# Kernel tuning notes

Measured on AMD Instinct MI355X. Metric: run time of the kernel, lower is better.

The kernel has to match this reference:

```python
import jax, jax.numpy as jnp
import numpy as np

B, Q, C = 16, 2048, 256
SCORE_THRESH = 0.05   # lowered from 0.7 so the mask is non-trivial with 256 classes
NMS_THRESH = 0.7
LABEL_OFFSET = 1e5    # batched_nms trick: offset boxes per class so cross-class IoU ~ 0


def box_cxcywh_to_xyxy(b):
    cx, cy, w, h = jnp.split(b, 4, axis=-1)
    return jnp.concatenate([cx - 0.5 * w, cy - 0.5 * h, cx + 0.5 * w, cy + 0.5 * h], axis=-1)


def pairwise_iou(boxes):
    # boxes: [N,4] xyxy -> iou: [N,N]
    area = jnp.clip(boxes[:, 2] - boxes[:, 0], 0) * jnp.clip(boxes[:, 3] - boxes[:, 1], 0)
    lt = jnp.maximum(boxes[:, None, :2], boxes[None, :, :2])
    rb = jnp.minimum(boxes[:, None, 2:], boxes[None, :, 2:])
    wh = jnp.clip(rb - lt, 0)
    inter = wh[..., 0] * wh[..., 1]
    union = area[:, None] + area[None, :] - inter
    return inter / jnp.maximum(union, 1e-6)


def nms_single(boxes, scores, labels, valid):
    # Emulates torchvision batched_nms with fixed-size (padded) output:
    # returns score-sorted boxes/scores/labels plus a boolean keep mask.
    n = boxes.shape[0]
    boxes_off = boxes + labels.astype(boxes.dtype)[:, None] * LABEL_OFFSET
    order = jnp.argsort(jnp.where(valid, scores, -jnp.inf))[::-1]
    b_off = boxes_off[order]
    s = scores[order]
    l = labels[order]
    v = valid[order]
    iou = pairwise_iou(b_off)  # [N,N], class-offset so only same-class overlap
    idx = jnp.arange(n)

    def step(keep, x):
        row, i = x  # row: iou of box i vs all
        sup = (row > NMS_THRESH) & (idx > i) & keep[i]
        return keep & ~sup, None

    keep, _ = jax.lax.scan(step, v, (iou, idx))
    return boxes[order], s, l, keep & v


def setup_inputs() -> dict:
    key = jax.random.key(0)
    k1, k2, k3 = jax.random.split(key, 3)
    pred_logits = jax.random.normal(k1, (B, Q, C), dtype=jnp.float32)
    pred_boxes = jax.random.uniform(k2, (B, Q, 4), dtype=jnp.float32)
    target_sizes = jax.random.randint(k3, (B, 2), 480, 1333, dtype=jnp.int32)
    return {"pred_logits": pred_logits, "pred_boxes": pred_boxes, "target_sizes": target_sizes}


def reference(pred_logits, pred_boxes, target_sizes):
    prob = jax.nn.softmax(pred_logits, axis=-1)
    cls_prob = prob[..., :-1]            # drop 'no-object' class
    scores = cls_prob.max(axis=-1)       # [B,Q]
    labels = cls_prob.argmax(axis=-1)    # [B,Q]
    boxes = box_cxcywh_to_xyxy(pred_boxes)
    ts = target_sizes.astype(boxes.dtype)
    img_h, img_w = ts[:, 0], ts[:, 1]
    scale = jnp.stack([img_w, img_h, img_w, img_h], axis=1)  # [B,4]
    boxes = boxes * scale[:, None, :]
    valid = scores >= SCORE_THRESH
    out_boxes, out_scores, out_labels, keep = jax.vmap(nms_single)(boxes, scores, labels, valid)
    return out_boxes, out_scores, out_labels, keep
```

## Files before the change

kernel.cpp:

```cpp
#include <hip/hip_runtime.h>
#include <math.h>

#define NB 16
#define BQ 2048
#define NC 256
#define NL 255

typedef unsigned long long u64;
typedef unsigned int u32;
typedef unsigned short u16;
typedef unsigned char u8;

__device__ __forceinline__ u32 ord_f32(float f) {
  u32 b = __float_as_uint(f);
  return (b & 0x80000000u) ? ~b : (b | 0x80000000u);
}

__global__ __launch_bounds__(256) void score_box_kernel(
    const float* __restrict__ logits,
    const float* __restrict__ pboxes,
    const int* __restrict__ tsz,
    float* __restrict__ out)
{
#pragma clang fp contract(off)
  const int lane = threadIdx.x & 63;
  const int g = lane & 15;
  const int wv = threadIdx.x >> 6;
  const int q = (blockIdx.x * 4 + wv) * 4 + (lane >> 4);
  const float* row = logits + (size_t)q * NC + g * 16;
  const float4 la = *reinterpret_cast<const float4*>(row);
  const float4 lb4 = *reinterpret_cast<const float4*>(row + 4);
  const float4 lc = *reinterpret_cast<const float4*>(row + 8);
  const float4 ld = *reinterpret_cast<const float4*>(row + 12);

  float m = fmaxf(fmaxf(fmaxf(la.x, la.y), fmaxf(la.z, la.w)),
           fmaxf(fmaxf(fmaxf(lb4.x, lb4.y), fmaxf(lb4.z, lb4.w)),
           fmaxf(fmaxf(fmaxf(lc.x, lc.y), fmaxf(lc.z, lc.w)),
                 fmaxf(fmaxf(ld.x, ld.y), fmaxf(ld.z, ld.w)))));
  #pragma unroll
  for (int d = 1; d < 16; d <<= 1) m = fmaxf(m, __shfl_xor(m, d));

  float4 ea, eb, ec, ed;
  ea.x = expf(la.x - m);  ea.y = expf(la.y - m);  ea.z = expf(la.z - m);  ea.w = expf(la.w - m);
  eb.x = expf(lb4.x - m); eb.y = expf(lb4.y - m); eb.z = expf(lb4.z - m); eb.w = expf(lb4.w - m);
  ec.x = expf(lc.x - m);  ec.y = expf(lc.y - m);  ec.z = expf(lc.z - m);  ec.w = expf(lc.w - m);
  ed.x = expf(ld.x - m);  ed.y = expf(ld.y - m);  ed.z = expf(ld.z - m);  ed.w = expf(ld.w - m);

  float s = (((ea.x + ea.y) + (ea.z + ea.w)) + ((eb.x + eb.y) + (eb.z + eb.w)))
          + (((ec.x + ec.y) + (ec.z + ec.w)) + ((ed.x + ed.y) + (ed.z + ed.w)));
  #pragma unroll
  for (int d = 1; d < 16; d <<= 1) s += __shfl_xor(s, d);

  const int c0 = g * 16;
  float bp = ea.x / s; int bc = c0;
  float p;
  p = ea.y / s; if (p > bp) { bp = p; bc = c0 + 1; }
  p = ea.z / s; if (p > bp) { bp = p; bc = c0 + 2; }
  p = ea.w / s; if (p > bp) { bp = p; bc = c0 + 3; }
  p = eb.x / s; if (p > bp) { bp = p; bc = c0 + 4; }
  p = eb.y / s; if (p > bp) { bp = p; bc = c0 + 5; }
  p = eb.z / s; if (p > bp) { bp = p; bc = c0 + 6; }
  p = eb.w / s; if (p > bp) { bp = p; bc = c0 + 7; }
  p = ec.x / s; if (p > bp) { bp = p; bc = c0 + 8; }
  p = ec.y / s; if (p > bp) { bp = p; bc = c0 + 9; }
  p = ec.z / s; if (p > bp) { bp = p; bc = c0 + 10; }
  p = ec.w / s; if (p > bp) { bp = p; bc = c0 + 11; }
  p = ed.x / s; if (p > bp) { bp = p; bc = c0 + 12; }
  p = ed.y / s; if (p > bp) { bp = p; bc = c0 + 13; }
  p = ed.z / s; if (p > bp) { bp = p; bc = c0 + 14; }
  p = ed.w / s; if (g != 15 && p > bp) { bp = p; bc = c0 + 15; }
  #pragma unroll
  for (int d = 1; d < 16; d <<= 1) {
    const float op = __shfl_xor(bp, d);
    const int   oc = __shfl_xor(bc, d);
    if (op > bp || (op == bp && oc < bc)) { bp = op; bc = oc; }
  }

  if (g == 0) {
    const int b = q >> 11;
    float hf = (float)tsz[b * 2 + 0];
    float wf = (float)tsz[b * 2 + 1];
    float4 pb = *reinterpret_cast<const float4*>(pboxes + (size_t)q * 4);
    float hw = 0.5f * pb.z, hh = 0.5f * pb.w;
    float4 ob;
    ob.x = (pb.x - hw) * wf;
    ob.y = (pb.y - hh) * hf;
    ob.z = (pb.x + hw) * wf;
    ob.w = (pb.y + hh) * hf;
    *reinterpret_cast<float4*>(out + (size_t)q * 4) = ob;
    out[NB * BQ * 4 + q] = bp;
    out[NB * BQ * 5 + q] = (float)bc;
  }
}

__global__ __launch_bounds__(1024) void sort_nms_kernel(float* __restrict__ out)
{
#pragma clang fp contract(off)
  __shared__ __align__(16) u64 cvk[BQ];
  __shared__ u32 cgt_a[BQ];
  __shared__ float4 bx[BQ];
  __shared__ float4 bxo[BQ];
  __shared__ float scr[BQ];
  __shared__ u8 lb[BQ];
  __shared__ u8 lbp[BQ];
  __shared__ u8 kp[BQ];
  __shared__ u16 sidx[BQ];
  __shared__ u16 gpos[BQ];
  __shared__ u16 hist[32 * 256];
  __shared__ u32 tot[256];
  __shared__ u32 scn[256];
  __shared__ u32 wval[16], winv[16];

  const int b = blockIdx.x;
  const int tid = threadIdx.x;
  const int lane = tid & 63;
  const int wv = tid >> 6;
  float* boxes_g  = out + (size_t)b * BQ * 4;
  float* scores_g = out + NB * BQ * 4 + (size_t)b * BQ;
  float* labels_g = out + NB * BQ * 5 + (size_t)b * BQ;
  float* keep_g   = out + NB * BQ * 6 + (size_t)b * BQ;

  const int q0 = 2 * tid;
  float2 s2 = *reinterpret_cast<const float2*>(scores_g + q0);
  float2 lf = *reinterpret_cast<const float2*>(labels_g + q0);
  float4 bb0 = *reinterpret_cast<const float4*>(boxes_g + (size_t)q0 * 4);
  float4 bb1 = *reinterpret_cast<const float4*>(boxes_g + (size_t)q0 * 4 + 4);
  scr[q0] = s2.x; scr[q0 + 1] = s2.y;
  const u32 l0 = (u32)(int)lf.x, l1 = (u32)(int)lf.y;
  lb[q0] = (u8)l0; lb[q0 + 1] = (u8)l1;
  bx[q0] = bb0; bx[q0 + 1] = bb1;
  cgt_a[tid] = 0; cgt_a[tid + 1024] = 0;
  reinterpret_cast<u32*>(hist)[tid]        = 0;
  reinterpret_cast<u32*>(hist)[tid + 1024] = 0;
  reinterpret_cast<u32*>(hist)[tid + 2048] = 0;
  reinterpret_cast<u32*>(hist)[tid + 3072] = 0;
  const bool v0 = (s2.x >= 0.05f), v1 = (s2.y >= 0.05f);
  const u64 f0 = ((u64)(v0 ? ord_f32(s2.x) : 0x007FFFFFu) << 32) | ((u32)q0 << 8) | l0;
  const u64 f1 = ((u64)(v1 ? ord_f32(s2.y) : 0x007FFFFFu) << 32) | ((u32)(q0 + 1) << 8) | l1;
  const u64 b0 = __ballot(v0), b1 = __ballot(v1);
  if (lane == 0) {
    const u32 c = (u32)(__popcll(b0) + __popcll(b1));
    wval[wv] = c;
    winv[wv] = 128u - c;
  }
  __syncthreads();

  int nv = 0, voff = 0, ioff = 0;
  #pragma unroll
  for (int w = 0; w < 16; ++w) {
    const int c = (int)wval[w];
    nv += c;
    if (w < wv) { voff += c; ioff += (int)winv[w]; }
  }
  const int tinv = BQ - nv;
  const u64 below = (1ull << lane) - 1ull;
  const int vr0 = voff + (int)__popcll(b0 & below) + (int)__popcll(b1 & below);
  const int ir0 = ioff + (int)__popcll(~b0 & below) + (int)__popcll(~b1 & below);
  const int vr1 = vr0 + (v0 ? 1 : 0);
  const int ir1 = ir0 + (v0 ? 0 : 1);
  if (v0) cvk[vr0] = f0;
  else { const int ip = nv + (tinv - 1 - ir0); sidx[ip] = (u16)q0; lbp[ip] = 255; kp[ip] = 0; }
  if (v1) cvk[vr1] = f1;
  else { const int ip = nv + (tinv - 1 - ir1); sidx[ip] = (u16)(q0 + 1); lbp[ip] = 255; kp[ip] = 0; }
  __syncthreads();

  const int nvc = (nv + 63) >> 6;
  const int nitems = nvc * nvc;
  for (int it = wv; it < nitems; it += 16) {
    const int sc_ = it / nvc;
    const int jc = it - sc_ * nvc;
    const int slot = (sc_ << 6) + lane;
    const u64 ki = cvk[slot];
    const int j0 = jc << 6;
    int lim = nv - j0; if (lim > 64) lim = 64;
    const u64* jp = &cvk[j0];
    int cgt = 0;
    #pragma unroll 8
    for (int l = 0; l < lim; ++l) cgt += (jp[l] > ki) ? 1 : 0;
    if (slot < nv && cgt) atomicAdd(&cgt_a[slot], (u32)cgt);
  }
  __syncthreads();

  for (int slot = tid; slot < nv; slot += 1024) {
    const u64 ki = cvk[slot];
    const u32 p = cgt_a[slot];
    const u32 oi = (u32)(ki >> 8) & (BQ - 1);
    const u32 li = (u32)ki & 255u;
    sidx[p] = (u16)oi;
    lbp[p] = (u8)li;
    const float lc = (float)li * 100000.0f;
    const float4 A = bx[oi];
    float4 Ao;
    Ao.x = A.x + lc; Ao.y = A.y + lc; Ao.z = A.z + lc; Ao.w = A.w + lc;
    bxo[p] = Ao;
  }
  __syncthreads();

  int lA, lB; u32 rA, rB;
  {
    const int p = tid;
    lA = (int)lbp[p];
    u64 m = ~0ull;
    #pragma unroll
    for (int bt = 0; bt < 8; ++bt) {
      const u64 vb = __ballot(((lA >> bt) & 1));
      m &= ((lA >> bt) & 1) ? vb : ~vb;
    }
    rA = (u32)__popcll(m & below);
    if (lane == 63 - __builtin_clzll(m)) hist[(p >> 6) * 256 + lA] = (u16)__popcll(m);
  }
  {
    const int p = tid + 1024;
    lB = (int)lbp[p];
    u64 m = ~0ull;
    #pragma unroll
    for (int bt = 0; bt < 8; ++bt) {
      const u64 vb = __ballot(((lB >> bt) & 1));
      m &= ((lB >> bt) & 1) ? vb : ~vb;
    }
    rB = (u32)__popcll(m & below);
    if (lane == 63 - __builtin_clzll(m)) hist[(p >> 6) * 256 + lB] = (u16)__popcll(m);
  }
  __syncthreads();

  if (tid < 256) {
    u32 run = 0;
    #pragma unroll
    for (int c = 0; c < 32; ++c) {
      const u32 v = hist[c * 256 + tid];
      hist[c * 256 + tid] = (u16)run;
      run += v;
    }
    tot[tid] = run;
  }
  __syncthreads();

  if (tid < 64) {
    u32 carry = 0;
    for (int seg = 0; seg < 4; ++seg) {
      const int l = seg * 64 + tid;
      u32 x = tot[l];
      #pragma unroll
      for (int s = 1; s < 64; s <<= 1) {
        const u32 y = __shfl_up(x, s, 64);
        if (lane >= s) x += y;
      }
      scn[l] = x + carry;
      carry += __shfl(x, 63, 64);
    }
  }
  __syncthreads();

  u32 gA, gB;
  {
    const int p = tid;
    const u32 st = (lA == 0) ? 0u : scn[lA - 1];
    gA = (u32)hist[(p >> 6) * 256 + lA] + rA;
    gpos[st + gA] = (u16)p;
  }
  {
    const int p = tid + 1024;
    const u32 st = (lB == 0) ? 0u : scn[lB - 1];
    gB = (u32)hist[(p >> 6) * 256 + lB] + rB;
    gpos[st + gB] = (u16)p;
  }
  __syncthreads();

  #pragma unroll
  for (int half = 0; half < 2; ++half) {
    const int p = tid + half * 1024;
    const int l = half ? lB : lA;
    const u32 g = half ? gB : gA;
    if (p < nv && g < 64) {
      const u32 st = (l == 0) ? 0u : scn[l - 1];
      const float4 Ao = bxo[p];
      const float areaA = fmaxf(Ao.z - Ao.x, 0.0f) * fmaxf(Ao.w - Ao.y, 0.0f);
      u64 m = 0;
      for (u32 r = 0; r < g; ++r) {
        const int p2 = gpos[st + r];
        const float4 Bo = bxo[p2];
        const float areaB = fmaxf(Bo.z - Bo.x, 0.0f) * fmaxf(Bo.w - Bo.y, 0.0f);
        const float ltx = fmaxf(Ao.x, Bo.x), lty = fmaxf(Ao.y, Bo.y);
        const float rbx = fminf(Ao.z, Bo.z), rby = fminf(Ao.w, Bo.w);
        const float iw = fmaxf(rbx - ltx, 0.0f), ih = fmaxf(rby - lty, 0.0f);
        const float inter = iw * ih;
        const float uni = (areaA + areaB) - inter;
        const float iou = inter / fmaxf(uni, 1e-6f);
        if (iou > 0.7f) m |= (1ull << r);
      }
      cvk[st + g] = m;
    }
  }
  __syncthreads();

  if (tid < NL) {
    const int k = (int)tot[tid];
    if (k > 0) {
      const int st = (tid == 0) ? 0 : (int)scn[tid - 1];
      if (k <= 64) {
        u64 kept = 0;
        for (int r = 0; r < k; ++r) {
          const u64 m = cvk[st + r];
          const int keep = ((m & kept) == 0) ? 1 : 0;
          kept |= (u64)keep << r;
          kp[gpos[st + r]] = (u8)keep;
        }
      } else {
        for (int a = 0; a < k; ++a) {
          const int p = gpos[st + a];
          const float4 Ao = bxo[p];
          const float areaA = fmaxf(Ao.z - Ao.x, 0.0f) * fmaxf(Ao.w - Ao.y, 0.0f);
          int keep = 1;
          for (int e = 0; e < a; ++e) {
            const int p2 = gpos[st + e];
            if (!kp[p2]) continue;
            const float4 Bo = bxo[p2];
            const float areaB = fmaxf(Bo.z - Bo.x, 0.0f) * fmaxf(Bo.w - Bo.y, 0.0f);
            const float ltx = fmaxf(Ao.x, Bo.x), lty = fmaxf(Ao.y, Bo.y);
            const float rbx = fminf(Ao.z, Bo.z), rby = fminf(Ao.w, Bo.w);
            const float iw = fmaxf(rbx - ltx, 0.0f), ih = fmaxf(rby - lty, 0.0f);
            const float inter = iw * ih;
            const float uni = (areaA + areaB) - inter;
            const float iou = inter / fmaxf(uni, 1e-6f);
            if (iou > 0.7f) { keep = 0; break; }
          }
          kp[p] = (u8)keep;
        }
      }
    }
  }
  __syncthreads();

  {
    const int p = tid;
    const u32 oi = sidx[p];
    *reinterpret_cast<float4*>(boxes_g + (size_t)p * 4) = bx[oi];
    scores_g[p] = scr[oi];
    labels_g[p] = (float)lb[oi];
    keep_g[p]   = kp[p] ? 1.0f : 0.0f;
  }
  {
    const int p = tid + 1024;
    const u32 oi = sidx[p];
    *reinterpret_cast<float4*>(boxes_g + (size_t)p * 4) = bx[oi];
    scores_g[p] = scr[oi];
    labels_g[p] = (float)lb[oi];
    keep_g[p]   = kp[p] ? 1.0f : 0.0f;
  }
}

extern "C" void kernel_launch(void* const* d_in, const int* in_sizes, int n_in,
                              void* d_out, int out_size, void* d_ws, size_t ws_size,
                              hipStream_t stream) {
  const float* logits = (const float*)d_in[0];
  const float* pboxes = (const float*)d_in[1];
  const int*   tsz    = (const int*)d_in[2];
  float* out = (float*)d_out;
  score_box_kernel<<<NB * BQ / 16, 256, 0, stream>>>(logits, pboxes, tsz, out);
  sort_nms_kernel<<<NB, 1024, 0, stream>>>(out);
}
```

Measured before the change: 30.00 us.

## Write sorted outputs early, skip invalid tail in label grouping, parallelize hist scan

Invalid (below-threshold) entries are now written straight to global memory during compaction, and valid sorted outputs are written right after the sort. This removes the final output pass and the scr/lb/kp shared arrays. Label-histogram grouping now only covers the valid prefix, rounded up to a wave, and the per-label column prefix scan uses four threads per label instead of one. Keep flags go straight to global from the NMS stage, with a small per-group keep array for the fallback path. The trade-off is scattered global writes and a layout that depends on the kernel reading and writing the same buffer in place.

```diff
diff --git a/kernel.cpp b/kernel.cpp
--- a/kernel.cpp
+++ b/kernel.cpp
@@ -100,12 +100,11 @@
   __shared__ u32 cgt_a[BQ];
   __shared__ float4 bx[BQ];
   __shared__ float4 bxo[BQ];
-  __shared__ float scr[BQ];
-  __shared__ u8 lb[BQ];
+  __shared__ u32 sco[BQ];
   __shared__ u8 lbp[BQ];
-  __shared__ u8 kp[BQ];
   __shared__ u16 sidx[BQ];
   __shared__ u16 gpos[BQ];
+  __shared__ u8 grpk[BQ];
   __shared__ u16 hist[32 * 256];
   __shared__ u32 tot[256];
   __shared__ u32 scn[256];
@@ -125,9 +124,7 @@
   float2 lf = *reinterpret_cast<const float2*>(labels_g + q0);
   float4 bb0 = *reinterpret_cast<const float4*>(boxes_g + (size_t)q0 * 4);
   float4 bb1 = *reinterpret_cast<const float4*>(boxes_g + (size_t)q0 * 4 + 4);
-  scr[q0] = s2.x; scr[q0 + 1] = s2.y;
   const u32 l0 = (u32)(int)lf.x, l1 = (u32)(int)lf.y;
-  lb[q0] = (u8)l0; lb[q0 + 1] = (u8)l1;
   bx[q0] = bb0; bx[q0 + 1] = bb1;
   cgt_a[tid] = 0; cgt_a[tid + 1024] = 0;
   reinterpret_cast<u32*>(hist)[tid]        = 0;
@@ -135,8 +132,8 @@
   reinterpret_cast<u32*>(hist)[tid + 2048] = 0;
   reinterpret_cast<u32*>(hist)[tid + 3072] = 0;
   const bool v0 = (s2.x >= 0.05f), v1 = (s2.y >= 0.05f);
-  const u64 f0 = ((u64)(v0 ? ord_f32(s2.x) : 0x007FFFFFu) << 32) | ((u32)q0 << 8) | l0;
-  const u64 f1 = ((u64)(v1 ? ord_f32(s2.y) : 0x007FFFFFu) << 32) | ((u32)(q0 + 1) << 8) | l1;
+  const u64 f0 = ((u64)ord_f32(s2.x) << 32) | ((u32)q0 << 8) | l0;
+  const u64 f1 = ((u64)ord_f32(s2.y) << 32) | ((u32)(q0 + 1) << 8) | l1;
   const u64 b0 = __ballot(v0), b1 = __ballot(v1);
   if (lane == 0) {
     const u32 c = (u32)(__popcll(b0) + __popcll(b1));
@@ -159,25 +156,35 @@
   const int vr1 = vr0 + (v0 ? 1 : 0);
   const int ir1 = ir0 + (v0 ? 0 : 1);
   if (v0) cvk[vr0] = f0;
-  else { const int ip = nv + (tinv - 1 - ir0); sidx[ip] = (u16)q0; lbp[ip] = 255; kp[ip] = 0; }
+  else {
+    const int ip = nv + (tinv - 1 - ir0);
+    *reinterpret_cast<float4*>(boxes_g + (size_t)ip * 4) = bb0;
+    scores_g[ip] = s2.x; labels_g[ip] = lf.x; keep_g[ip] = 0.0f;
+  }
   if (v1) cvk[vr1] = f1;
-  else { const int ip = nv + (tinv - 1 - ir1); sidx[ip] = (u16)(q0 + 1); lbp[ip] = 255; kp[ip] = 0; }
+  else {
+    const int ip = nv + (tinv - 1 - ir1);
+    *reinterpret_cast<float4*>(boxes_g + (size_t)ip * 4) = bb1;
+    scores_g[ip] = s2.y; labels_g[ip] = lf.y; keep_g[ip] = 0.0f;
+  }
   __syncthreads();
 
   const int nvc = (nv + 63) >> 6;
-  const int nitems = nvc * nvc;
-  for (int it = wv; it < nitems; it += 16) {
-    const int sc_ = it / nvc;
-    const int jc = it - sc_ * nvc;
-    const int slot = (sc_ << 6) + lane;
-    const u64 ki = cvk[slot];
-    const int j0 = jc << 6;
-    int lim = nv - j0; if (lim > 64) lim = 64;
-    const u64* jp = &cvk[j0];
-    int cgt = 0;
-    #pragma unroll 8
-    for (int l = 0; l < lim; ++l) cgt += (jp[l] > ki) ? 1 : 0;
-    if (slot < nv && cgt) atomicAdd(&cgt_a[slot], (u32)cgt);
+  {
+    const int nitems = nvc * nvc;
+    for (int it = wv; it < nitems; it += 16) {
+      const int sc_ = it / nvc;
+      const int jc = it - sc_ * nvc;
+      const int slot = (sc_ << 6) + lane;
+      const u64 ki = cvk[slot];
+      const int j0 = jc << 6;
+      int lim = nv - j0; if (lim > 64) lim = 64;
+      const u64* jp = &cvk[j0];
+      int cgt = 0;
+      #pragma unroll 8
+      for (int l = 0; l < lim; ++l) cgt += (jp[l] > ki) ? 1 : 0;
+      if (slot < nv && cgt) atomicAdd(&cgt_a[slot], (u32)cgt);
+    }
   }
   __syncthreads();
 
@@ -188,50 +195,71 @@
     const u32 li = (u32)ki & 255u;
     sidx[p] = (u16)oi;
     lbp[p] = (u8)li;
+    sco[p] = (u32)(ki >> 32) & 0x7FFFFFFFu;
     const float lc = (float)li * 100000.0f;
     const float4 A = bx[oi];
     float4 Ao;
     Ao.x = A.x + lc; Ao.y = A.y + lc; Ao.z = A.z + lc; Ao.w = A.w + lc;
     bxo[p] = Ao;
   }
-  __syncthreads();
-
-  int lA, lB; u32 rA, rB;
+  for (int p = nv + tid; p < (nvc << 6); p += 1024) lbp[p] = 255;
+  __syncthreads();
+
+  int lA = 255, lB = 255; u32 rA = 0, rB = 0;
   {
     const int p = tid;
-    lA = (int)lbp[p];
-    u64 m = ~0ull;
+    if (p < (nvc << 6)) {
+      lA = (int)lbp[p];
+      u64 m = ~0ull;
+      #pragma unroll
+      for (int bt = 0; bt < 8; ++bt) {
+        const u64 vb = __ballot(((lA >> bt) & 1));
+        m &= ((lA >> bt) & 1) ? vb : ~vb;
+      }
+      rA = (u32)__popcll(m & below);
+      if (lane == 63 - __builtin_clzll(m)) hist[(p >> 6) * 256 + lA] = (u16)__popcll(m);
+    }
+  }
+  {
+    const int p = tid + 1024;
+    if (p < (nvc << 6)) {
+      lB = (int)lbp[p];
+      u64 m = ~0ull;
+      #pragma unroll
+      for (int bt = 0; bt < 8; ++bt) {
+        const u64 vb = __ballot(((lB >> bt) & 1));
+        m &= ((lB >> bt) & 1) ? vb : ~vb;
+      }
+      rB = (u32)__popcll(m & below);
+      if (lane == 63 - __builtin_clzll(m)) hist[(p >> 6) * 256 + lB] = (u16)__popcll(m);
+    }
+  }
+  for (int p = tid; p < nv; p += 1024) {
+    const u32 oi = sidx[p];
+    *reinterpret_cast<float4*>(boxes_g + (size_t)p * 4) = bx[oi];
+    scores_g[p] = __uint_as_float(sco[p]);
+    labels_g[p] = (float)lbp[p];
+  }
+  __syncthreads();
+
+  {
+    const int l = tid >> 2, t4 = tid & 3;
+    u16 v0_[8]; u32 sum = 0;
     #pragma unroll
-    for (int bt = 0; bt < 8; ++bt) {
-      const u64 vb = __ballot(((lA >> bt) & 1));
-      m &= ((lA >> bt) & 1) ? vb : ~vb;
-    }
-    rA = (u32)__popcll(m & below);
-    if (lane == 63 - __builtin_clzll(m)) hist[(p >> 6) * 256 + lA] = (u16)__popcll(m);
-  }
-  {
-    const int p = tid + 1024;
-    lB = (int)lbp[p];
-    u64 m = ~0ull;
+    for (int i = 0; i < 8; ++i) {
+      v0_[i] = hist[(t4 * 8 + i) * 256 + l];
+      sum += v0_[i];
+    }
+    u32 x = sum;
+    u32 y = __shfl_up(x, 1, 64); if (t4 >= 1) x += y;
+    y = __shfl_up(x, 2, 64);     if (t4 >= 2) x += y;
+    u32 run = x - sum;
     #pragma unroll
-    for (int bt = 0; bt < 8; ++bt) {
-      const u64 vb = __ballot(((lB >> bt) & 1));
-      m &= ((lB >> bt) & 1) ? vb : ~vb;
-    }
-    rB = (u32)__popcll(m & below);
-    if (lane == 63 - __builtin_clzll(m)) hist[(p >> 6) * 256 + lB] = (u16)__popcll(m);
-  }
-  __syncthreads();
-
-  if (tid < 256) {
-    u32 run = 0;
-    #pragma unroll
-    for (int c = 0; c < 32; ++c) {
-      const u32 v = hist[c * 256 + tid];
-      hist[c * 256 + tid] = (u16)run;
-      run += v;
-    }
-    tot[tid] = run;
+    for (int i = 0; i < 8; ++i) {
+      hist[(t4 * 8 + i) * 256 + l] = (u16)run;
+      run += v0_[i];
+    }
+    if (t4 == 3) tot[l] = x;
   }
   __syncthreads();
 
@@ -251,18 +279,22 @@
   }
   __syncthreads();
 
-  u32 gA, gB;
+  u32 gA = ~0u, gB = ~0u;
   {
     const int p = tid;
-    const u32 st = (lA == 0) ? 0u : scn[lA - 1];
-    gA = (u32)hist[(p >> 6) * 256 + lA] + rA;
-    gpos[st + gA] = (u16)p;
+    if (lA != 255) {
+      const u32 st = (lA == 0) ? 0u : scn[lA - 1];
+      gA = (u32)hist[(p >> 6) * 256 + lA] + rA;
+      gpos[st + gA] = (u16)p;
+    }
   }
   {
     const int p = tid + 1024;
-    const u32 st = (lB == 0) ? 0u : scn[lB - 1];
-    gB = (u32)hist[(p >> 6) * 256 + lB] + rB;
-    gpos[st + gB] = (u16)p;
+    if (lB != 255) {
+      const u32 st = (lB == 0) ? 0u : scn[lB - 1];
+      gB = (u32)hist[(p >> 6) * 256 + lB] + rB;
+      gpos[st + gB] = (u16)p;
+    }
   }
   __syncthreads();
 
@@ -303,7 +335,7 @@
           const u64 m = cvk[st + r];
           const int keep = ((m & kept) == 0) ? 1 : 0;
           kept |= (u64)keep << r;
-          kp[gpos[st + r]] = (u8)keep;
+          keep_g[gpos[st + r]] = keep ? 1.0f : 0.0f;
         }
       } else {
         for (int a = 0; a < k; ++a) {
@@ -312,8 +344,8 @@
           const float areaA = fmaxf(Ao.z - Ao.x, 0.0f) * fmaxf(Ao.w - Ao.y, 0.0f);
           int keep = 1;
           for (int e = 0; e < a; ++e) {
+            if (!grpk[st + e]) continue;
             const int p2 = gpos[st + e];
-            if (!kp[p2]) continue;
             const float4 Bo = bxo[p2];
             const float areaB = fmaxf(Bo.z - Bo.x, 0.0f) * fmaxf(Bo.w - Bo.y, 0.0f);
             const float ltx = fmaxf(Ao.x, Bo.x), lty = fmaxf(Ao.y, Bo.y);
@@ -324,28 +356,11 @@
             const float iou = inter / fmaxf(uni, 1e-6f);
             if (iou > 0.7f) { keep = 0; break; }
           }
-          kp[p] = (u8)keep;
+          grpk[st + a] = (u8)keep;
+          keep_g[p] = keep ? 1.0f : 0.0f;
         }
       }
     }
-  }
-  __syncthreads();
-
-  {
-    const int p = tid;
-    const u32 oi = sidx[p];
-    *reinterpret_cast<float4*>(boxes_g + (size_t)p * 4) = bx[oi];
-    scores_g[p] = scr[oi];
-    labels_g[p] = (float)lb[oi];
-    keep_g[p]   = kp[p] ? 1.0f : 0.0f;
-  }
-  {
-    const int p = tid + 1024;
-    const u32 oi = sidx[p];
-    *reinterpret_cast<float4*>(boxes_g + (size_t)p * 4) = bx[oi];
-    scores_g[p] = scr[oi];
-    labels_g[p] = (float)lb[oi];
-    keep_g[p]   = kp[p] ? 1.0f : 0.0f;
   }
 }
 
```

Result: no change. 30.16 us (+0.5%).
